# Optimization experiments

Hardware: AMD Instinct MI355X
Metric: run time of the kernel (lower is better)

The kernel has to match this reference:

```python
import jax, jax.numpy as jnp
import numpy as np

N = 50000
E = 300000
NEG_SLOPE = 0.2
EPS = 1e-16


def setup_inputs() -> dict:
    key = jax.random.key(0)
    ks = jax.random.split(key, 12)
    x = jax.random.normal(ks[0], (N, 27), dtype=jnp.float32)
    edge_index = jax.random.randint(ks[1], (2, E), 0, N, dtype=jnp.int64)
    # layer 1: in=27 -> heads1=4, dim=64
    W1 = jax.random.normal(ks[2], (27, 4 * 64), dtype=jnp.float32) * 0.1
    a_src1 = jax.random.normal(ks[3], (4, 64), dtype=jnp.float32) * 0.1
    a_dst1 = jax.random.normal(ks[4], (4, 64), dtype=jnp.float32) * 0.1
    b1 = jnp.zeros((4 * 64,), dtype=jnp.float32)
    # layer 2: in=256 -> heads2=2, dim=64
    W2 = jax.random.normal(ks[5], (256, 2 * 64), dtype=jnp.float32) * 0.05
    a_src2 = jax.random.normal(ks[6], (2, 64), dtype=jnp.float32) * 0.1
    a_dst2 = jax.random.normal(ks[7], (2, 64), dtype=jnp.float32) * 0.1
    b2 = jnp.zeros((2 * 64,), dtype=jnp.float32)
    # final linear: 128 -> 1
    Wfc = jax.random.normal(ks[8], (128, 1), dtype=jnp.float32) * 0.05
    bfc = jnp.zeros((1,), dtype=jnp.float32)
    return {"x": x, "edge_index": edge_index, "W1": W1, "a_src1": a_src1,
            "a_dst1": a_dst1, "b1": b1, "W2": W2, "a_src2": a_src2,
            "a_dst2": a_dst2, "b2": b2, "Wfc": Wfc, "bfc": bfc}


def gat_layer(x, src, dst, W, a_src, a_dst, b, heads, dim):
    # h: [N, H, D]
    h = (x @ W).reshape(N, heads, dim)
    # per-node attention half-scores: [N, H]
    s_src = jnp.einsum('nhd,hd->nh', h, a_src)
    s_dst = jnp.einsum('nhd,hd->nh', h, a_dst)
    # per-edge logits (gather) + leaky relu: [E', H]
    logits = jax.nn.leaky_relu(s_src[src] + s_dst[dst], negative_slope=NEG_SLOPE)
    # segment softmax over incoming edges at each destination node
    m = jax.ops.segment_max(logits, dst, num_segments=N)  # [N, H]
    m = jnp.where(jnp.isfinite(m), m, 0.0)
    e = jnp.exp(logits - m[dst])
    z = jax.ops.segment_sum(e, dst, num_segments=N)  # [N, H]
    alpha = e / (z[dst] + EPS)
    # weighted scatter-aggregate of source features
    out = jax.ops.segment_sum(h[src] * alpha[:, :, None], dst, num_segments=N)
    return out.reshape(N, heads * dim) + b


def reference(x, edge_index, W1, a_src1, a_dst1, b1, W2, a_src2, a_dst2, b2, Wfc, bfc):
    # add self-loops (PyG GATConv default add_self_loops=True)
    loops = jnp.arange(N, dtype=edge_index.dtype)
    src = jnp.concatenate([edge_index[0], loops])
    dst = jnp.concatenate([edge_index[1], loops])
    h = gat_layer(x, src, dst, W1, a_src1, a_dst1, b1, heads=4, dim=64)
    h = jax.nn.elu(h)
    h = gat_layer(h, src, dst, W2, a_src2, a_dst2, b2, heads=2, dim=64)
    h = jax.nn.elu(h)
    out = h @ Wfc + bfc
    return jax.nn.sigmoid(out)
```

## Files before the change

kernel.cpp:

```cpp
#include <hip/hip_runtime.h>
#include <math.h>

#define N_NODES 50000
#define E_EDGES 300000
#define E_TOT   350000
#define NEG 0.2f
#define EPS 1e-16f
#define CAP 32

typedef __attribute__((ext_vector_type(8))) short bf16x8;
typedef __attribute__((ext_vector_type(4))) float f32x4;

__device__ __forceinline__ float leaky(float x) { return x > 0.f ? x : NEG * x; }
__device__ __forceinline__ short f2bf(float v) {
    unsigned u = __float_as_uint(v);
    u += 0x7fffu + ((u >> 16) & 1u);
    return (short)(u >> 16);
}
__device__ __forceinline__ float bflo(unsigned u) { return __uint_as_float(u << 16); }
__device__ __forceinline__ float bfhi(unsigned u) { return __uint_as_float(u & 0xffff0000u); }
__device__ __forceinline__ unsigned bfpack(short a, short b) {
    return (unsigned)(unsigned short)a | ((unsigned)(unsigned short)b << 16);
}

__global__ __launch_bounds__(256) void k_scatter_s1(const int* __restrict__ ei,
        int* __restrict__ cnt, int* __restrict__ eidx,
        const float* __restrict__ x,
        const float* __restrict__ W1, const float* __restrict__ as1,
        const float* __restrict__ ad1, const float* __restrict__ W2,
        float* __restrict__ s1, short* __restrict__ xb,
        short* __restrict__ W1b, short* __restrict__ W2bT) {
    __shared__ float wsvL[216];
    int t = blockIdx.x * 256 + threadIdx.x;
    if (threadIdx.x < 216) {
        int k = threadIdx.x >> 3, j = threadIdx.x & 7;
        const float* av = (j < 4) ? (as1 + j * 64) : (ad1 + (j - 4) * 64);
        const float* wr = W1 + k * 256 + ((j & 3) * 64);
        float s = 0.f;
        #pragma unroll
        for (int d = 0; d < 64; ++d) s += wr[d] * av[d];
        wsvL[threadIdx.x] = s;
    }
    if (t < E_TOT) {
        int s = (t < E_EDGES) ? ei[t] : (t - E_EDGES);
        int d = (t < E_EDGES) ? ei[E_EDGES + t] : (t - E_EDGES);
        int pos = atomicAdd(&cnt[d], 1);
        if (pos < CAP) eidx[d * CAP + pos] = s;
    }
    if (t < 32768) {
        int col = t >> 8, k = t & 255;
        W2bT[t] = f2bf(W2[k * 128 + col]);
    }
    if (t < 8192) {
        int h = t >> 11, col = (t >> 5) & 63, k = t & 31;
        W1b[t] = f2bf(k < 27 ? W1[k * 256 + h * 64 + col] : 0.f);
    }
    __syncthreads();
    if (t < N_NODES * 8) {
        int n = t >> 3, j = t & 7;
        float s = 0.f;
        #pragma unroll
        for (int k = 0; k < 27; ++k) s += x[n * 27 + k] * wsvL[k * 8 + j];
        s1[t] = s;
        int c0 = j * 4;
        short p0 = f2bf(c0 + 0 < 27 ? x[n * 27 + c0 + 0] : 0.f);
        short p1 = f2bf(c0 + 1 < 27 ? x[n * 27 + c0 + 1] : 0.f);
        short p2 = f2bf(c0 + 2 < 27 ? x[n * 27 + c0 + 2] : 0.f);
        short p3 = f2bf(c0 + 3 < 27 ? x[n * 27 + c0 + 3] : 0.f);
        uint2 wv;
        wv.x = bfpack(p0, p1);
        wv.y = bfpack(p2, p3);
        *(uint2*)(xb + n * 32 + c0) = wv;
    }
}

__global__ __launch_bounds__(256) void k_fused1(const int* __restrict__ cnt,
        const int* __restrict__ eidx, const short* __restrict__ xb,
        const float* __restrict__ s1, const short* __restrict__ W1b,
        const short* __restrict__ W2bT, const float* __restrict__ b1,
        const float* __restrict__ as2, const float* __restrict__ ad2,
        short* __restrict__ h2b, float* __restrict__ s2) {
    __shared__ short LDSx[4 * 16 * 32];
    __shared__ short O[16 * 264];
    __shared__ float P[4][2][16];
    int w = threadIdx.x >> 6, l = threadIdx.x & 63;
    int n0 = blockIdx.x * 16;
    f32x4 z4 = {0.f, 0.f, 0.f, 0.f};

    {
        int g = threadIdx.x >> 4;
        int q = threadIdx.x & 15;
        int n = n0 + g;
        int beg = n * CAP;
        int espec = eidx[beg + q];
        int deg = min(cnt[n], CAP);
        int myi = (q < deg) ? espec : n;
        float4 sdv = *(const float4*)(s1 + n * 8 + 4);
        float a0 = 0.f, a1 = 0.f, a2 = 0.f, a3 = 0.f;
        float b0 = 0.f, b1v = 0.f, b2v = 0.f, b3 = 0.f;
        float z0 = 0.f, z1 = 0.f, z2 = 0.f, z3 = 0.f;
        float4 svq = *(const float4*)(s1 + myi * 8);
        float me0 = __expf(leaky(svq.x + sdv.x));
        float me1 = __expf(leaky(svq.y + sdv.y));
        float me2 = __expf(leaky(svq.z + sdv.z));
        float me3 = __expf(leaky(svq.w + sdv.w));
        int degw = deg;
        degw = max(degw, __shfl_xor(degw, 16));
        degw = max(degw, __shfl_xor(degw, 32));
        if (degw <= 16) {
            int lw = deg - 1;
            for (int i = 0; i < degw; i += 4) {
                bool m0 = i < deg, m1 = (i + 1) < deg;
                bool m2 = (i + 2) < deg, m3 = (i + 3) < deg;
                int j0 = m0 ? i : lw;
                int j1 = m1 ? i + 1 : lw;
                int j2 = m2 ? i + 2 : lw;
                int j3 = m3 ? i + 3 : lw;
                float g0 = m0 ? 1.f : 0.f, g1 = m1 ? 1.f : 0.f;
                float g2 = m2 ? 1.f : 0.f, g3 = m3 ? 1.f : 0.f;
                int s0 = __shfl(myi, j0, 16);
                int s1i = __shfl(myi, j1, 16);
                int s2i = __shfl(myi, j2, 16);
                int s3 = __shfl(myi, j3, 16);
                float e00 = g0 * __shfl(me0, j0, 16);
                float e01 = g0 * __shfl(me1, j0, 16);
                float e02 = g0 * __shfl(me2, j0, 16);
                float e03 = g0 * __shfl(me3, j0, 16);
                float e10 = g1 * __shfl(me0, j1, 16);
                float e11 = g1 * __shfl(me1, j1, 16);
                float e12 = g1 * __shfl(me2, j1, 16);
                float e13 = g1 * __shfl(me3, j1, 16);
                float e20 = g2 * __shfl(me0, j2, 16);
                float e21 = g2 * __shfl(me1, j2, 16);
                float e22 = g2 * __shfl(me2, j2, 16);
                float e23 = g2 * __shfl(me3, j2, 16);
                float e30 = g3 * __shfl(me0, j3, 16);
                float e31 = g3 * __shfl(me1, j3, 16);
                float e32 = g3 * __shfl(me2, j3, 16);
                float e33 = g3 * __shfl(me3, j3, 16);
                unsigned xv0 = *(const unsigned*)(xb + s0 * 32 + 2 * q);
                unsigned xv1 = *(const unsigned*)(xb + s1i * 32 + 2 * q);
                unsigned xv2 = *(const unsigned*)(xb + s2i * 32 + 2 * q);
                unsigned xv3 = *(const unsigned*)(xb + s3 * 32 + 2 * q);
                float xa0 = bflo(xv0), xc0 = bfhi(xv0);
                float xa1 = bflo(xv1), xc1 = bfhi(xv1);
                float xa2 = bflo(xv2), xc2 = bfhi(xv2);
                float xa3 = bflo(xv3), xc3 = bfhi(xv3);
                z0 += e00 + e10 + e20 + e30;
                z1 += e01 + e11 + e21 + e31;
                z2 += e02 + e12 + e22 + e32;
                z3 += e03 + e13 + e23 + e33;
                a0 += e00 * xa0 + e10 * xa1 + e20 * xa2 + e30 * xa3;
                a1 += e01 * xa0 + e11 * xa1 + e21 * xa2 + e31 * xa3;
                a2 += e02 * xa0 + e12 * xa1 + e22 * xa2 + e32 * xa3;
                a3 += e03 * xa0 + e13 * xa1 + e23 * xa2 + e33 * xa3;
                b0  += e00 * xc0 + e10 * xc1 + e20 * xc2 + e30 * xc3;
                b1v += e01 * xc0 + e11 * xc1 + e21 * xc2 + e31 * xc3;
                b2v += e02 * xc0 + e12 * xc1 + e22 * xc2 + e32 * xc3;
                b3  += e03 * xc0 + e13 * xc1 + e23 * xc2 + e33 * xc3;
            }
        } else {
            int last = beg + deg - 1;
            for (int i = 0; i < deg; i += 4) {
                bool m1 = (i + 1) < deg, m2 = (i + 2) < deg, m3 = (i + 3) < deg;
                int p0 = beg + i;
                int p1 = m1 ? p0 + 1 : last;
                int p2 = m2 ? p0 + 2 : last;
                int p3 = m3 ? p0 + 3 : last;
                int s0 = eidx[p0];
                int s1i = eidx[p1];
                int s2i = eidx[p2];
                int s3 = eidx[p3];
                float4 sv0 = *(const float4*)(s1 + s0 * 8);
                float4 sv1 = *(const float4*)(s1 + s1i * 8);
                float4 sv2 = *(const float4*)(s1 + s2i * 8);
                float4 sv3 = *(const float4*)(s1 + s3 * 8);
                unsigned xv0 = *(const unsigned*)(xb + s0 * 32 + 2 * q);
                unsigned xv1 = *(const unsigned*)(xb + s1i * 32 + 2 * q);
                unsigned xv2 = *(const unsigned*)(xb + s2i * 32 + 2 * q);
                unsigned xv3 = *(const unsigned*)(xb + s3 * 32 + 2 * q);
                float xa0 = bflo(xv0), xc0 = bfhi(xv0);
                float xa1 = bflo(xv1), xc1 = bfhi(xv1);
                float xa2 = bflo(xv2), xc2 = bfhi(xv2);
                float xa3 = bflo(xv3), xc3 = bfhi(xv3);
                float g1 = m1 ? 1.f : 0.f, g2 = m2 ? 1.f : 0.f, g3 = m3 ? 1.f : 0.f;
                float e00 = __expf(leaky(sv0.x + sdv.x));
                float e01 = __expf(leaky(sv0.y + sdv.y));
                float e02 = __expf(leaky(sv0.z + sdv.z));
                float e03 = __expf(leaky(sv0.w + sdv.w));
                float e10 = g1 * __expf(leaky(sv1.x + sdv.x));
                float e11 = g1 * __expf(leaky(sv1.y + sdv.y));
                float e12 = g1 * __expf(leaky(sv1.z + sdv.z));
                float e13 = g1 * __expf(leaky(sv1.w + sdv.w));
                float e20 = g2 * __expf(leaky(sv2.x + sdv.x));
                float e21 = g2 * __expf(leaky(sv2.y + sdv.y));
                float e22 = g2 * __expf(leaky(sv2.z + sdv.z));
                float e23 = g2 * __expf(leaky(sv2.w + sdv.w));
                float e30 = g3 * __expf(leaky(sv3.x + sdv.x));
                float e31 = g3 * __expf(leaky(sv3.y + sdv.y));
                float e32 = g3 * __expf(leaky(sv3.z + sdv.z));
                float e33 = g3 * __expf(leaky(sv3.w + sdv.w));
                z0 += e00 + e10 + e20 + e30;
                z1 += e01 + e11 + e21 + e31;
                z2 += e02 + e12 + e22 + e32;
                z3 += e03 + e13 + e23 + e33;
                a0 += e00 * xa0 + e10 * xa1 + e20 * xa2 + e30 * xa3;
                a1 += e01 * xa0 + e11 * xa1 + e21 * xa2 + e31 * xa3;
                a2 += e02 * xa0 + e12 * xa1 + e22 * xa2 + e32 * xa3;
                a3 += e03 * xa0 + e13 * xa1 + e23 * xa2 + e33 * xa3;
                b0  += e00 * xc0 + e10 * xc1 + e20 * xc2 + e30 * xc3;
                b1v += e01 * xc0 + e11 * xc1 + e21 * xc2 + e31 * xc3;
                b2v += e02 * xc0 + e12 * xc1 + e22 * xc2 + e32 * xc3;
                b3  += e03 * xc0 + e13 * xc1 + e23 * xc2 + e33 * xc3;
            }
        }
        float i0 = 1.f / (z0 + EPS), i1 = 1.f / (z1 + EPS);
        float i2 = 1.f / (z2 + EPS), i3 = 1.f / (z3 + EPS);
        int c2 = 2 * q;
        LDSx[0 * 512 + g * 32 + c2] = f2bf(a0 * i0);
        LDSx[1 * 512 + g * 32 + c2] = f2bf(a1 * i1);
        LDSx[2 * 512 + g * 32 + c2] = f2bf(a2 * i2);
        LDSx[3 * 512 + g * 32 + c2] = f2bf(a3 * i3);
        LDSx[0 * 512 + g * 32 + c2 + 1] = f2bf(b0 * i0);
        LDSx[1 * 512 + g * 32 + c2 + 1] = f2bf(b1v * i1);
        LDSx[2 * 512 + g * 32 + c2 + 1] = f2bf(b2v * i2);
        LDSx[3 * 512 + g * 32 + c2 + 1] = f2bf(b3 * i3);
    }
    __syncthreads();

    int lane16 = l & 15, quad = l >> 4;
    {
        bf16x8 a = *(const bf16x8*)&LDSx[w * 512 + lane16 * 32 + quad * 8];
        f32x4 cacc[4];
        #pragma unroll
        for (int nt = 0; nt < 4; ++nt) {
            bf16x8 b = *(const bf16x8*)&W1b[w * 2048 + (nt * 16 + lane16) * 32 + quad * 8];
            cacc[nt] = __builtin_amdgcn_mfma_f32_16x16x32_bf16(a, b, z4, 0, 0, 0);
        }
        #pragma unroll
        for (int nt = 0; nt < 4; ++nt) {
            int col = w * 64 + nt * 16 + lane16;
            float bb = b1[col];
            #pragma unroll
            for (int r2 = 0; r2 < 4; ++r2) {
                float v = cacc[nt][r2] + bb;
                v = v > 0.f ? v : __expf(v) - 1.f;
                O[(quad * 4 + r2) * 264 + col] = f2bf(v);
            }
        }
    }
    __syncthreads();

    f32x4 acc2[2];
    acc2[0] = z4; acc2[1] = z4;
    for (int k0 = 0; k0 < 256; k0 += 32) {
        bf16x8 a2 = *(const bf16x8*)&O[lane16 * 264 + k0 + quad * 8];
        #pragma unroll
        for (int j = 0; j < 2; ++j) {
            int ct = 2 * w + j;
            bf16x8 b2 = *(const bf16x8*)&W2bT[(ct * 16 + lane16) * 256 + k0 + quad * 8];
            acc2[j] = __builtin_amdgcn_mfma_f32_16x16x32_bf16(a2, b2, acc2[j], 0, 0, 0);
        }
    }
    float ps[4] = {0.f, 0.f, 0.f, 0.f}, pd[4] = {0.f, 0.f, 0.f, 0.f};
    #pragma unroll
    for (int j = 0; j < 2; ++j) {
        int col = (2 * w + j) * 16 + lane16;
        float a_s = as2[col], a_d = ad2[col];
        #pragma unroll
        for (int r2 = 0; r2 < 4; ++r2) {
            ps[r2] += acc2[j][r2] * a_s;
            pd[r2] += acc2[j][r2] * a_d;
            h2b[(n0 + quad * 4 + r2) * 128 + col] = f2bf(acc2[j][r2]);
        }
    }
    #pragma unroll
    for (int off = 1; off <= 8; off <<= 1)
        #pragma unroll
        for (int r2 = 0; r2 < 4; ++r2) {
            ps[r2] += __shfl_xor(ps[r2], off);
            pd[r2] += __shfl_xor(pd[r2], off);
        }
    if (lane16 == 0) {
        #pragma unroll
        for (int r2 = 0; r2 < 4; ++r2) {
            P[w][0][quad * 4 + r2] = ps[r2];
            P[w][1][quad * 4 + r2] = pd[r2];
        }
    }
    __syncthreads();
    if (threadIdx.x < 32) {
        int m = threadIdx.x & 15, hd = threadIdx.x >> 4;
        s2[(n0 + m) * 4 + hd]     = P[2 * hd][0][m] + P[2 * hd + 1][0][m];
        s2[(n0 + m) * 4 + 2 + hd] = P[2 * hd][1][m] + P[2 * hd + 1][1][m];
    }
}

__global__ __launch_bounds__(256) void k_agg2_csr(const int* __restrict__ cnt,
        const int* __restrict__ eidx, const float* __restrict__ s2,
        const short* __restrict__ h2b, const float* __restrict__ b2,
        const float* __restrict__ Wfc, const float* __restrict__ bfc,
        float* __restrict__ out) {
    int g = threadIdx.x >> 4;
    int q = threadIdx.x & 15;
    int n = blockIdx.x * 16 + g;
    int beg = n * CAP;
    int espec = eidx[beg + q];
    int deg = min(cnt[n], CAP);
    int myi = (q < deg) ? espec : n;
    int h = q >> 3;
    float2 sdv = *(const float2*)(s2 + n * 4 + 2);
    float4 accA = make_float4(0.f, 0.f, 0.f, 0.f);
    float4 accB = make_float4(0.f, 0.f, 0.f, 0.f);
    float z = 0.f;
    float2 svq = *(const float2*)(s2 + myi * 4);
    float mea = __expf(leaky(svq.x + sdv.x));
    float meb = __expf(leaky(svq.y + sdv.y));
    int degw = deg;
    degw = max(degw, __shfl_xor(degw, 16));
    degw = max(degw, __shfl_xor(degw, 32));
    if (degw <= 16) {
        int lw = deg - 1;
        for (int i = 0; i < degw; i += 4) {
            bool m0 = i < deg, m1 = (i + 1) < deg;
            bool m2 = (i + 2) < deg, m3 = (i + 3) < deg;
            int j0 = m0 ? i : lw;
            int j1 = m1 ? i + 1 : lw;
            int j2 = m2 ? i + 2 : lw;
            int j3 = m3 ? i + 3 : lw;
            int a0 = __shfl(myi, j0, 16);
            int a1 = __shfl(myi, j1, 16);
            int a2 = __shfl(myi, j2, 16);
            int a3 = __shfl(myi, j3, 16);
            float ea0 = __shfl(mea, j0, 16), eb0 = __shfl(meb, j0, 16);
            float ea1 = __shfl(mea, j1, 16), eb1 = __shfl(meb, j1, 16);
            float ea2 = __shfl(mea, j2, 16), eb2 = __shfl(meb, j2, 16);
            float ea3 = __shfl(mea, j3, 16), eb3 = __shfl(meb, j3, 16);
            float e0 = (m0 ? 1.f : 0.f) * (h ? eb0 : ea0);
            float e1 = (m1 ? 1.f : 0.f) * (h ? eb1 : ea1);
            float e2 = (m2 ? 1.f : 0.f) * (h ? eb2 : ea2);
            float e3 = (m3 ? 1.f : 0.f) * (h ? eb3 : ea3);
            uint4 v0 = *(const uint4*)(h2b + a0 * 128 + q * 8);
            uint4 v1 = *(const uint4*)(h2b + a1 * 128 + q * 8);
            uint4 v2 = *(const uint4*)(h2b + a2 * 128 + q * 8);
            uint4 v3 = *(const uint4*)(h2b + a3 * 128 + q * 8);
            z += e0 + e1 + e2 + e3;
            accA.x += e0 * bflo(v0.x) + e1 * bflo(v1.x) + e2 * bflo(v2.x) + e3 * bflo(v3.x);
            accA.y += e0 * bfhi(v0.x) + e1 * bfhi(v1.x) + e2 * bfhi(v2.x) + e3 * bfhi(v3.x);
            accA.z += e0 * bflo(v0.y) + e1 * bflo(v1.y) + e2 * bflo(v2.y) + e3 * bflo(v3.y);
            accA.w += e0 * bfhi(v0.y) + e1 * bfhi(v1.y) + e2 * bfhi(v2.y) + e3 * bfhi(v3.y);
            accB.x += e0 * bflo(v0.z) + e1 * bflo(v1.z) + e2 * bflo(v2.z) + e3 * bflo(v3.z);
            accB.y += e0 * bfhi(v0.z) + e1 * bfhi(v1.z) + e2 * bfhi(v2.z) + e3 * bfhi(v3.z);
            accB.z += e0 * bflo(v0.w) + e1 * bflo(v1.w) + e2 * bflo(v2.w) + e3 * bflo(v3.w);
            accB.w += e0 * bfhi(v0.w) + e1 * bfhi(v1.w) + e2 * bfhi(v2.w) + e3 * bfhi(v3.w);
        }
    } else {
        float sd = h ? sdv.y : sdv.x;
        int i = 0;
        for (; i + 4 <= deg; i += 4) {
            int a0 = eidx[beg + i], a1 = eidx[beg + i + 1];
            int a2 = eidx[beg + i + 2], a3 = eidx[beg + i + 3];
            float e0 = __expf(leaky(s2[a0 * 4 + h] + sd));
            float e1 = __expf(leaky(s2[a1 * 4 + h] + sd));
            float e2 = __expf(leaky(s2[a2 * 4 + h] + sd));
            float e3 = __expf(leaky(s2[a3 * 4 + h] + sd));
            uint4 v0 = *(const uint4*)(h2b + a0 * 128 + q * 8);
            uint4 v1 = *(const uint4*)(h2b + a1 * 128 + q * 8);
            uint4 v2 = *(const uint4*)(h2b + a2 * 128 + q * 8);
            uint4 v3 = *(const uint4*)(h2b + a3 * 128 + q * 8);
            z += e0 + e1 + e2 + e3;
            accA.x += e0 * bflo(v0.x) + e1 * bflo(v1.x) + e2 * bflo(v2.x) + e3 * bflo(v3.x);
            accA.y += e0 * bfhi(v0.x) + e1 * bfhi(v1.x) + e2 * bfhi(v2.x) + e3 * bfhi(v3.x);
            accA.z += e0 * bflo(v0.y) + e1 * bflo(v1.y) + e2 * bflo(v2.y) + e3 * bflo(v3.y);
            accA.w += e0 * bfhi(v0.y) + e1 * bfhi(v1.y) + e2 * bfhi(v2.y) + e3 * bfhi(v3.y);
            accB.x += e0 * bflo(v0.z) + e1 * bflo(v1.z) + e2 * bflo(v2.z) + e3 * bflo(v3.z);
            accB.y += e0 * bfhi(v0.z) + e1 * bfhi(v1.z) + e2 * bfhi(v2.z) + e3 * bfhi(v3.z);
            accB.z += e0 * bflo(v0.w) + e1 * bflo(v1.w) + e2 * bflo(v2.w) + e3 * bflo(v3.w);
            accB.w += e0 * bfhi(v0.w) + e1 * bfhi(v1.w) + e2 * bfhi(v2.w) + e3 * bfhi(v3.w);
        }
        for (; i < deg; ++i) {
            int a0 = eidx[beg + i];
            float e0 = __expf(leaky(s2[a0 * 4 + h] + sd));
            uint4 v0 = *(const uint4*)(h2b + a0 * 128 + q * 8);
            z += e0;
            accA.x += e0 * bflo(v0.x); accA.y += e0 * bfhi(v0.x);
            accA.z += e0 * bflo(v0.y); accA.w += e0 * bfhi(v0.y);
            accB.x += e0 * bflo(v0.z); accB.y += e0 * bfhi(v0.z);
            accB.z += e0 * bflo(v0.w); accB.w += e0 * bfhi(v0.w);
        }
    }
    float inv = 1.f / (z + EPS);
    int c0 = q * 8;
    float p = 0.f;
    float va[8] = {accA.x, accA.y, accA.z, accA.w, accB.x, accB.y, accB.z, accB.w};
    #pragma unroll
    for (int j = 0; j < 8; ++j) {
        float v = va[j] * inv + b2[c0 + j];
        v = v > 0.f ? v : __expf(v) - 1.f;
        p += v * Wfc[c0 + j];
    }
    #pragma unroll
    for (int off = 1; off <= 8; off <<= 1) p += __shfl_xor(p, off);
    if (q == 0) out[n] = 1.f / (1.f + __expf(-(p + bfc[0])));
}

extern "C" void kernel_launch(void* const* d_in, const int* in_sizes, int n_in,
                              void* d_out, int out_size, void* d_ws, size_t ws_size,
                              hipStream_t stream) {
    const float* x   = (const float*)d_in[0];
    const int*   ei  = (const int*)d_in[1];
    const float* W1  = (const float*)d_in[2];
    const float* as1 = (const float*)d_in[3];
    const float* ad1 = (const float*)d_in[4];
    const float* b1  = (const float*)d_in[5];
    const float* W2  = (const float*)d_in[6];
    const float* as2 = (const float*)d_in[7];
    const float* ad2 = (const float*)d_in[8];
    const float* b2  = (const float*)d_in[9];
    const float* Wfc = (const float*)d_in[10];
    const float* bfc = (const float*)d_in[11];
    float* out = (float*)d_out;

    float* f = (float*)d_ws;
    short* h2b   = (short*)f;
    float* s1    = f + 3200000;
    float* s2    = f + 3600000;
    int*   cnt   = (int*)(f + 3810000);
    int*   eidx  = (int*)(f + 3870000);
    short* W1b   = (short*)(f + 5500000);
    short* W2bT  = (short*)(f + 5510000);
    short* xb    = (short*)(f + 5530000);

    hipMemsetAsync(cnt, 0, N_NODES * sizeof(int), stream);

    k_scatter_s1<<<1563, 256, 0, stream>>>(ei, cnt, eidx, x, W1, as1, ad1, W2,
                                           s1, xb, W1b, W2bT);

    k_fused1<<<3125, 256, 0, stream>>>(cnt, eidx, xb, s1, W1b, W2bT, b1,
                                       as2, ad2, h2b, s2);

    k_agg2_csr<<<3125, 256, 0, stream>>>(cnt, eidx, s2, h2b, b2, Wfc, bfc, out);
}
```

Baseline: 168.9 us.

## Split fused layer-1 kernel into gather kernel and 32-row MFMA dense kernel

The fused kernel that gathered neighbour features and then ran both MFMA GEMMs is split in two. The gather kernel writes the normalized per-head aggregates to a padded global bf16 buffer. The dense kernel then processes 32 nodes per block, so each W1/W2 fragment load feeds two MFMAs. This decouples the latency-bound gather from the compute-bound dense work and improves weight reuse. In exchange it adds an extra kernel launch and a global round trip for the aggregated features, plus padding writes.

```diff
diff --git a/kernel.cpp b/kernel.cpp
--- a/kernel.cpp
+++ b/kernel.cpp
@@ -2,11 +2,13 @@
 #include <math.h>
 
 #define N_NODES 50000
+#define N_PAD   50016
 #define E_EDGES 300000
 #define E_TOT   350000
 #define NEG 0.2f
 #define EPS 1e-16f
 #define CAP 32
+#define PLANE (N_PAD * 32)
 
 typedef __attribute__((ext_vector_type(8))) short bf16x8;
 typedef __attribute__((ext_vector_type(4))) float f32x4;
@@ -74,168 +76,174 @@
     }
 }
 
-__global__ __launch_bounds__(256) void k_fused1(const int* __restrict__ cnt,
+__global__ __launch_bounds__(256) void k_gather1(const int* __restrict__ cnt,
         const int* __restrict__ eidx, const short* __restrict__ xb,
-        const float* __restrict__ s1, const short* __restrict__ W1b,
-        const short* __restrict__ W2bT, const float* __restrict__ b1,
-        const float* __restrict__ as2, const float* __restrict__ ad2,
-        short* __restrict__ h2b, float* __restrict__ s2) {
-    __shared__ short LDSx[4 * 16 * 32];
-    __shared__ short O[16 * 264];
-    __shared__ float P[4][2][16];
+        const float* __restrict__ s1, short* __restrict__ xagg) {
+    int g = threadIdx.x >> 4;
+    int q = threadIdx.x & 15;
+    int n = blockIdx.x * 16 + g;
+    int c2 = 2 * q;
+    if (n >= N_NODES) {
+        if (n < N_PAD) {
+            *(unsigned*)(xagg + 0 * PLANE + n * 32 + c2) = 0u;
+            *(unsigned*)(xagg + 1 * PLANE + n * 32 + c2) = 0u;
+            *(unsigned*)(xagg + 2 * PLANE + n * 32 + c2) = 0u;
+            *(unsigned*)(xagg + 3 * PLANE + n * 32 + c2) = 0u;
+        }
+        return;
+    }
+    int beg = n * CAP;
+    int espec = eidx[beg + q];
+    int deg = min(cnt[n], CAP);
+    int myi = (q < deg) ? espec : n;
+    float4 sdv = *(const float4*)(s1 + n * 8 + 4);
+    float a0 = 0.f, a1 = 0.f, a2 = 0.f, a3 = 0.f;
+    float b0 = 0.f, b1v = 0.f, b2v = 0.f, b3 = 0.f;
+    float z0 = 0.f, z1 = 0.f, z2 = 0.f, z3 = 0.f;
+    float4 svq = *(const float4*)(s1 + myi * 8);
+    float me0 = __expf(leaky(svq.x + sdv.x));
+    float me1 = __expf(leaky(svq.y + sdv.y));
+    float me2 = __expf(leaky(svq.z + sdv.z));
+    float me3 = __expf(leaky(svq.w + sdv.w));
+    int degw = deg;
+    degw = max(degw, __shfl_xor(degw, 16));
+    degw = max(degw, __shfl_xor(degw, 32));
+    if (degw <= 16) {
+        int lw = deg - 1;
+        for (int i = 0; i < degw; i += 4) {
+            bool m0 = i < deg, m1 = (i + 1) < deg;
+            bool m2 = (i + 2) < deg, m3 = (i + 3) < deg;
+            int j0 = m0 ? i : lw;
+            int j1 = m1 ? i + 1 : lw;
+            int j2 = m2 ? i + 2 : lw;
+            int j3 = m3 ? i + 3 : lw;
+            float g0 = m0 ? 1.f : 0.f, g1 = m1 ? 1.f : 0.f;
+            float g2 = m2 ? 1.f : 0.f, g3 = m3 ? 1.f : 0.f;
+            int s0 = __shfl(myi, j0, 16);
+            int s1i = __shfl(myi, j1, 16);
+            int s2i = __shfl(myi, j2, 16);
+            int s3 = __shfl(myi, j3, 16);
+            float e00 = g0 * __shfl(me0, j0, 16);
+            float e01 = g0 * __shfl(me1, j0, 16);
+            float e02 = g0 * __shfl(me2, j0, 16);
+            float e03 = g0 * __shfl(me3, j0, 16);
+            float e10 = g1 * __shfl(me0, j1, 16);
+            float e11 = g1 * __shfl(me1, j1, 16);
+            float e12 = g1 * __shfl(me2, j1, 16);
+            float e13 = g1 * __shfl(me3, j1, 16);
+            float e20 = g2 * __shfl(me0, j2, 16);
+            float e21 = g2 * __shfl(me1, j2, 16);
+            float e22 = g2 * __shfl(me2, j2, 16);
+            float e23 = g2 * __shfl(me3, j2, 16);
+            float e30 = g3 * __shfl(me0, j3, 16);
+            float e31 = g3 * __shfl(me1, j3, 16);
+            float e32 = g3 * __shfl(me2, j3, 16);
+            float e33 = g3 * __shfl(me3, j3, 16);
+            unsigned xv0 = *(const unsigned*)(xb + s0 * 32 + 2 * q);
+            unsigned xv1 = *(const unsigned*)(xb + s1i * 32 + 2 * q);
+            unsigned xv2 = *(const unsigned*)(xb + s2i * 32 + 2 * q);
+            unsigned xv3 = *(const unsigned*)(xb + s3 * 32 + 2 * q);
+            float xa0 = bflo(xv0), xc0 = bfhi(xv0);
+            float xa1 = bflo(xv1), xc1 = bfhi(xv1);
+            float xa2 = bflo(xv2), xc2 = bfhi(xv2);
+            float xa3 = bflo(xv3), xc3 = bfhi(xv3);
+            z0 += e00 + e10 + e20 + e30;
+            z1 += e01 + e11 + e21 + e31;
+            z2 += e02 + e12 + e22 + e32;
+            z3 += e03 + e13 + e23 + e33;
+            a0 += e00 * xa0 + e10 * xa1 + e20 * xa2 + e30 * xa3;
+            a1 += e01 * xa0 + e11 * xa1 + e21 * xa2 + e31 * xa3;
+            a2 += e02 * xa0 + e12 * xa1 + e22 * xa2 + e32 * xa3;
+            a3 += e03 * xa0 + e13 * xa1 + e23 * xa2 + e33 * xa3;
+            b0  += e00 * xc0 + e10 * xc1 + e20 * xc2 + e30 * xc3;
+            b1v += e01 * xc0 + e11 * xc1 + e21 * xc2 + e31 * xc3;
+            b2v += e02 * xc0 + e12 * xc1 + e22 * xc2 + e32 * xc3;
+            b3  += e03 * xc0 + e13 * xc1 + e23 * xc2 + e33 * xc3;
+        }
+    } else {
+        int last = beg + deg - 1;
+        for (int i = 0; i < deg; i += 4) {
+            bool m1 = (i + 1) < deg, m2 = (i + 2) < deg, m3 = (i + 3) < deg;
+            int p0 = beg + i;
+            int p1 = m1 ? p0 + 1 : last;
+            int p2 = m2 ? p0 + 2 : last;
+            int p3 = m3 ? p0 + 3 : last;
+            int s0 = eidx[p0];
+            int s1i = eidx[p1];
+            int s2i = eidx[p2];
+            int s3 = eidx[p3];
+            float4 sv0 = *(const float4*)(s1 + s0 * 8);
+            float4 sv1 = *(const float4*)(s1 + s1i * 8);
+            float4 sv2 = *(const float4*)(s1 + s2i * 8);
+            float4 sv3 = *(const float4*)(s1 + s3 * 8);
+            unsigned xv0 = *(const unsigned*)(xb + s0 * 32 + 2 * q);
+            unsigned xv1 = *(const unsigned*)(xb + s1i * 32 + 2 * q);
+            unsigned xv2 = *(const unsigned*)(xb + s2i * 32 + 2 * q);
+            unsigned xv3 = *(const unsigned*)(xb + s3 * 32 + 2 * q);
+            float xa0 = bflo(xv0), xc0 = bfhi(xv0);
+            float xa1 = bflo(xv1), xc1 = bfhi(xv1);
+            float xa2 = bflo(xv2), xc2 = bfhi(xv2);
+            float xa3 = bflo(xv3), xc3 = bfhi(xv3);
+            float g1 = m1 ? 1.f : 0.f, g2 = m2 ? 1.f : 0.f, g3 = m3 ? 1.f : 0.f;
+            float e00 = __expf(leaky(sv0.x + sdv.x));
+            float e01 = __expf(leaky(sv0.y + sdv.y));
+            float e02 = __expf(leaky(sv0.z + sdv.z));
+            float e03 = __expf(leaky(sv0.w + sdv.w));
+            float e10 = g1 * __expf(leaky(sv1.x + sdv.x));
+            float e11 = g1 * __expf(leaky(sv1.y + sdv.y));
+            float e12 = g1 * __expf(leaky(sv1.z + sdv.z));
+            float e13 = g1 * __expf(leaky(sv1.w + sdv.w));
+            float e20 = g2 * __expf(leaky(sv2.x + sdv.x));
+            float e21 = g2 * __expf(leaky(sv2.y + sdv.y));
+            float e22 = g2 * __expf(leaky(sv2.z + sdv.z));
+            float e23 = g2 * __expf(leaky(sv2.w + sdv.w));
+            float e30 = g3 * __expf(leaky(sv3.x + sdv.x));
+            float e31 = g3 * __expf(leaky(sv3.y + sdv.y));
+            float e32 = g3 * __expf(leaky(sv3.z + sdv.z));
+            float e33 = g3 * __expf(leaky(sv3.w + sdv.w));
+            z0 += e00 + e10 + e20 + e30;
+            z1 += e01 + e11 + e21 + e31;
+            z2 += e02 + e12 + e22 + e32;
+            z3 += e03 + e13 + e23 + e33;
+            a0 += e00 * xa0 + e10 * xa1 + e20 * xa2 + e30 * xa3;
+            a1 += e01 * xa0 + e11 * xa1 + e21 * xa2 + e31 * xa3;
+            a2 += e02 * xa0 + e12 * xa1 + e22 * xa2 + e32 * xa3;
+            a3 += e03 * xa0 + e13 * xa1 + e23 * xa2 + e33 * xa3;
+            b0  += e00 * xc0 + e10 * xc1 + e20 * xc2 + e30 * xc3;
+            b1v += e01 * xc0 + e11 * xc1 + e21 * xc2 + e31 * xc3;
+            b2v += e02 * xc0 + e12 * xc1 + e22 * xc2 + e32 * xc3;
+            b3  += e03 * xc0 + e13 * xc1 + e23 * xc2 + e33 * xc3;
+        }
+    }
+    float i0 = 1.f / (z0 + EPS), i1 = 1.f / (z1 + EPS);
+    float i2 = 1.f / (z2 + EPS), i3 = 1.f / (z3 + EPS);
+    *(unsigned*)(xagg + 0 * PLANE + n * 32 + c2) = bfpack(f2bf(a0 * i0), f2bf(b0 * i0));
+    *(unsigned*)(xagg + 1 * PLANE + n * 32 + c2) = bfpack(f2bf(a1 * i1), f2bf(b1v * i1));
+    *(unsigned*)(xagg + 2 * PLANE + n * 32 + c2) = bfpack(f2bf(a2 * i2), f2bf(b2v * i2));
+    *(unsigned*)(xagg + 3 * PLANE + n * 32 + c2) = bfpack(f2bf(a3 * i3), f2bf(b3 * i3));
+}
+
+__global__ __launch_bounds__(256) void k_dense(const short* __restrict__ xagg,
+        const short* __restrict__ W1b, const short* __restrict__ W2bT,
+        const float* __restrict__ b1, const float* __restrict__ as2,
+        const float* __restrict__ ad2, short* __restrict__ h2b,
+        float* __restrict__ s2) {
+    __shared__ short O[32 * 264];
+    __shared__ float P[4][2][32];
     int w = threadIdx.x >> 6, l = threadIdx.x & 63;
-    int n0 = blockIdx.x * 16;
+    int lane16 = l & 15, quad = l >> 4;
+    int n0 = blockIdx.x * 32;
     f32x4 z4 = {0.f, 0.f, 0.f, 0.f};
 
     {
-        int g = threadIdx.x >> 4;
-        int q = threadIdx.x & 15;
-        int n = n0 + g;
-        int beg = n * CAP;
-        int espec = eidx[beg + q];
-        int deg = min(cnt[n], CAP);
-        int myi = (q < deg) ? espec : n;
-        float4 sdv = *(const float4*)(s1 + n * 8 + 4);
-        float a0 = 0.f, a1 = 0.f, a2 = 0.f, a3 = 0.f;
-        float b0 = 0.f, b1v = 0.f, b2v = 0.f, b3 = 0.f;
-        float z0 = 0.f, z1 = 0.f, z2 = 0.f, z3 = 0.f;
-        float4 svq = *(const float4*)(s1 + myi * 8);
-        float me0 = __expf(leaky(svq.x + sdv.x));
-        float me1 = __expf(leaky(svq.y + sdv.y));
-        float me2 = __expf(leaky(svq.z + sdv.z));
-        float me3 = __expf(leaky(svq.w + sdv.w));
-        int degw = deg;
-        degw = max(degw, __shfl_xor(degw, 16));
-        degw = max(degw, __shfl_xor(degw, 32));
-        if (degw <= 16) {
-            int lw = deg - 1;
-            for (int i = 0; i < degw; i += 4) {
-                bool m0 = i < deg, m1 = (i + 1) < deg;
-                bool m2 = (i + 2) < deg, m3 = (i + 3) < deg;
-                int j0 = m0 ? i : lw;
-                int j1 = m1 ? i + 1 : lw;
-                int j2 = m2 ? i + 2 : lw;
-                int j3 = m3 ? i + 3 : lw;
-                float g0 = m0 ? 1.f : 0.f, g1 = m1 ? 1.f : 0.f;
-                float g2 = m2 ? 1.f : 0.f, g3 = m3 ? 1.f : 0.f;
-                int s0 = __shfl(myi, j0, 16);
-                int s1i = __shfl(myi, j1, 16);
-                int s2i = __shfl(myi, j2, 16);
-                int s3 = __shfl(myi, j3, 16);
-                float e00 = g0 * __shfl(me0, j0, 16);
-                float e01 = g0 * __shfl(me1, j0, 16);
-                float e02 = g0 * __shfl(me2, j0, 16);
-                float e03 = g0 * __shfl(me3, j0, 16);
-                float e10 = g1 * __shfl(me0, j1, 16);
-                float e11 = g1 * __shfl(me1, j1, 16);
-                float e12 = g1 * __shfl(me2, j1, 16);
-                float e13 = g1 * __shfl(me3, j1, 16);
-                float e20 = g2 * __shfl(me0, j2, 16);
-                float e21 = g2 * __shfl(me1, j2, 16);
-                float e22 = g2 * __shfl(me2, j2, 16);
-                float e23 = g2 * __shfl(me3, j2, 16);
-                float e30 = g3 * __shfl(me0, j3, 16);
-                float e31 = g3 * __shfl(me1, j3, 16);
-                float e32 = g3 * __shfl(me2, j3, 16);
-                float e33 = g3 * __shfl(me3, j3, 16);
-                unsigned xv0 = *(const unsigned*)(xb + s0 * 32 + 2 * q);
-                unsigned xv1 = *(const unsigned*)(xb + s1i * 32 + 2 * q);
-                unsigned xv2 = *(const unsigned*)(xb + s2i * 32 + 2 * q);
-                unsigned xv3 = *(const unsigned*)(xb + s3 * 32 + 2 * q);
-                float xa0 = bflo(xv0), xc0 = bfhi(xv0);
-                float xa1 = bflo(xv1), xc1 = bfhi(xv1);
-                float xa2 = bflo(xv2), xc2 = bfhi(xv2);
-                float xa3 = bflo(xv3), xc3 = bfhi(xv3);
-                z0 += e00 + e10 + e20 + e30;
-                z1 += e01 + e11 + e21 + e31;
-                z2 += e02 + e12 + e22 + e32;
-                z3 += e03 + e13 + e23 + e33;
-                a0 += e00 * xa0 + e10 * xa1 + e20 * xa2 + e30 * xa3;
-                a1 += e01 * xa0 + e11 * xa1 + e21 * xa2 + e31 * xa3;
-                a2 += e02 * xa0 + e12 * xa1 + e22 * xa2 + e32 * xa3;
-                a3 += e03 * xa0 + e13 * xa1 + e23 * xa2 + e33 * xa3;
-                b0  += e00 * xc0 + e10 * xc1 + e20 * xc2 + e30 * xc3;
-                b1v += e01 * xc0 + e11 * xc1 + e21 * xc2 + e31 * xc3;
-                b2v += e02 * xc0 + e12 * xc1 + e22 * xc2 + e32 * xc3;
-                b3  += e03 * xc0 + e13 * xc1 + e23 * xc2 + e33 * xc3;
-            }
-        } else {
-            int last = beg + deg - 1;
-            for (int i = 0; i < deg; i += 4) {
-                bool m1 = (i + 1) < deg, m2 = (i + 2) < deg, m3 = (i + 3) < deg;
-                int p0 = beg + i;
-                int p1 = m1 ? p0 + 1 : last;
-                int p2 = m2 ? p0 + 2 : last;
-                int p3 = m3 ? p0 + 3 : last;
-                int s0 = eidx[p0];
-                int s1i = eidx[p1];
-                int s2i = eidx[p2];
-                int s3 = eidx[p3];
-                float4 sv0 = *(const float4*)(s1 + s0 * 8);
-                float4 sv1 = *(const float4*)(s1 + s1i * 8);
-                float4 sv2 = *(const float4*)(s1 + s2i * 8);
-                float4 sv3 = *(const float4*)(s1 + s3 * 8);
-                unsigned xv0 = *(const unsigned*)(xb + s0 * 32 + 2 * q);
-                unsigned xv1 = *(const unsigned*)(xb + s1i * 32 + 2 * q);
-                unsigned xv2 = *(const unsigned*)(xb + s2i * 32 + 2 * q);
-                unsigned xv3 = *(const unsigned*)(xb + s3 * 32 + 2 * q);
-                float xa0 = bflo(xv0), xc0 = bfhi(xv0);
-                float xa1 = bflo(xv1), xc1 = bfhi(xv1);
-                float xa2 = bflo(xv2), xc2 = bfhi(xv2);
-                float xa3 = bflo(xv3), xc3 = bfhi(xv3);
-                float g1 = m1 ? 1.f : 0.f, g2 = m2 ? 1.f : 0.f, g3 = m3 ? 1.f : 0.f;
-                float e00 = __expf(leaky(sv0.x + sdv.x));
-                float e01 = __expf(leaky(sv0.y + sdv.y));
-                float e02 = __expf(leaky(sv0.z + sdv.z));
-                float e03 = __expf(leaky(sv0.w + sdv.w));
-                float e10 = g1 * __expf(leaky(sv1.x + sdv.x));
-                float e11 = g1 * __expf(leaky(sv1.y + sdv.y));
-                float e12 = g1 * __expf(leaky(sv1.z + sdv.z));
-                float e13 = g1 * __expf(leaky(sv1.w + sdv.w));
-                float e20 = g2 * __expf(leaky(sv2.x + sdv.x));
-                float e21 = g2 * __expf(leaky(sv2.y + sdv.y));
-                float e22 = g2 * __expf(leaky(sv2.z + sdv.z));
-                float e23 = g2 * __expf(leaky(sv2.w + sdv.w));
-                float e30 = g3 * __expf(leaky(sv3.x + sdv.x));
-                float e31 = g3 * __expf(leaky(sv3.y + sdv.y));
-                float e32 = g3 * __expf(leaky(sv3.z + sdv.z));
-                float e33 = g3 * __expf(leaky(sv3.w + sdv.w));
-                z0 += e00 + e10 + e20 + e30;
-                z1 += e01 + e11 + e21 + e31;
-                z2 += e02 + e12 + e22 + e32;
-                z3 += e03 + e13 + e23 + e33;
-                a0 += e00 * xa0 + e10 * xa1 + e20 * xa2 + e30 * xa3;
-                a1 += e01 * xa0 + e11 * xa1 + e21 * xa2 + e31 * xa3;
-                a2 += e02 * xa0 + e12 * xa1 + e22 * xa2 + e32 * xa3;
-                a3 += e03 * xa0 + e13 * xa1 + e23 * xa2 + e33 * xa3;
-                b0  += e00 * xc0 + e10 * xc1 + e20 * xc2 + e30 * xc3;
-                b1v += e01 * xc0 + e11 * xc1 + e21 * xc2 + e31 * xc3;
-                b2v += e02 * xc0 + e12 * xc1 + e22 * xc2 + e32 * xc3;
-                b3  += e03 * xc0 + e13 * xc1 + e23 * xc2 + e33 * xc3;
-            }
-        }
-        float i0 = 1.f / (z0 + EPS), i1 = 1.f / (z1 + EPS);
-        float i2 = 1.f / (z2 + EPS), i3 = 1.f / (z3 + EPS);
-        int c2 = 2 * q;
-        LDSx[0 * 512 + g * 32 + c2] = f2bf(a0 * i0);
-        LDSx[1 * 512 + g * 32 + c2] = f2bf(a1 * i1);
-        LDSx[2 * 512 + g * 32 + c2] = f2bf(a2 * i2);
-        LDSx[3 * 512 + g * 32 + c2] = f2bf(a3 * i3);
-        LDSx[0 * 512 + g * 32 + c2 + 1] = f2bf(b0 * i0);
-        LDSx[1 * 512 + g * 32 + c2 + 1] = f2bf(b1v * i1);
-        LDSx[2 * 512 + g * 32 + c2 + 1] = f2bf(b2v * i2);
-        LDSx[3 * 512 + g * 32 + c2 + 1] = f2bf(b3 * i3);
-    }
-    __syncthreads();
-
-    int lane16 = l & 15, quad = l >> 4;
-    {
-        bf16x8 a = *(const bf16x8*)&LDSx[w * 512 + lane16 * 32 + quad * 8];
-        f32x4 cacc[4];
+        bf16x8 am0 = *(const bf16x8*)&xagg[w * PLANE + (n0 + lane16) * 32 + quad * 8];
+        bf16x8 am1 = *(const bf16x8*)&xagg[w * PLANE + (n0 + 16 + lane16) * 32 + quad * 8];
+        f32x4 c0[4], c1[4];
         #pragma unroll
         for (int nt = 0; nt < 4; ++nt) {
             bf16x8 b = *(const bf16x8*)&W1b[w * 2048 + (nt * 16 + lane16) * 32 + quad * 8];
-            cacc[nt] = __builtin_amdgcn_mfma_f32_16x16x32_bf16(a, b, z4, 0, 0, 0);
+            c0[nt] = __builtin_amdgcn_mfma_f32_16x16x32_bf16(am0, b, z4, 0, 0, 0);
+            c1[nt] = __builtin_amdgcn_mfma_f32_16x16x32_bf16(am1, b, z4, 0, 0, 0);
         }
         #pragma unroll
         for (int nt = 0; nt < 4; ++nt) {
@@ -243,56 +251,73 @@
             float bb = b1[col];
             #pragma unroll
             for (int r2 = 0; r2 < 4; ++r2) {
-                float v = cacc[nt][r2] + bb;
+                float v = c0[nt][r2] + bb;
                 v = v > 0.f ? v : __expf(v) - 1.f;
                 O[(quad * 4 + r2) * 264 + col] = f2bf(v);
+                float u = c1[nt][r2] + bb;
+                u = u > 0.f ? u : __expf(u) - 1.f;
+                O[(16 + quad * 4 + r2) * 264 + col] = f2bf(u);
             }
         }
     }
     __syncthreads();
 
-    f32x4 acc2[2];
-    acc2[0] = z4; acc2[1] = z4;
+    f32x4 acc[2][2];
+    acc[0][0] = z4; acc[0][1] = z4; acc[1][0] = z4; acc[1][1] = z4;
     for (int k0 = 0; k0 < 256; k0 += 32) {
-        bf16x8 a2 = *(const bf16x8*)&O[lane16 * 264 + k0 + quad * 8];
+        bf16x8 a0 = *(const bf16x8*)&O[lane16 * 264 + k0 + quad * 8];
+        bf16x8 a1 = *(const bf16x8*)&O[(16 + lane16) * 264 + k0 + quad * 8];
         #pragma unroll
         for (int j = 0; j < 2; ++j) {
             int ct = 2 * w + j;
             bf16x8 b2 = *(const bf16x8*)&W2bT[(ct * 16 + lane16) * 256 + k0 + quad * 8];
-            acc2[j] = __builtin_amdgcn_mfma_f32_16x16x32_bf16(a2, b2, acc2[j], 0, 0, 0);
-        }
-    }
-    float ps[4] = {0.f, 0.f, 0.f, 0.f}, pd[4] = {0.f, 0.f, 0.f, 0.f};
+            acc[0][j] = __builtin_amdgcn_mfma_f32_16x16x32_bf16(a0, b2, acc[0][j], 0, 0, 0);
+            acc[1][j] = __builtin_amdgcn_mfma_f32_16x16x32_bf16(a1, b2, acc[1][j], 0, 0, 0);
+        }
+    }
+    float ps[2][4] = {{0.f,0.f,0.f,0.f},{0.f,0.f,0.f,0.f}};
+    float pd[2][4] = {{0.f,0.f,0.f,0.f},{0.f,0.f,0.f,0.f}};
     #pragma unroll
     for (int j = 0; j < 2; ++j) {
         int col = (2 * w + j) * 16 + lane16;
         float a_s = as2[col], a_d = ad2[col];
         #pragma unroll
-        for (int r2 = 0; r2 < 4; ++r2) {
-            ps[r2] += acc2[j][r2] * a_s;
-            pd[r2] += acc2[j][r2] * a_d;
-            h2b[(n0 + quad * 4 + r2) * 128 + col] = f2bf(acc2[j][r2]);
+        for (int m = 0; m < 2; ++m) {
+            #pragma unroll
+            for (int r2 = 0; r2 < 4; ++r2) {
+                ps[m][r2] += acc[m][j][r2] * a_s;
+                pd[m][r2] += acc[m][j][r2] * a_d;
+                int row = n0 + m * 16 + quad * 4 + r2;
+                if (row < N_NODES) h2b[row * 128 + col] = f2bf(acc[m][j][r2]);
+            }
         }
     }
     #pragma unroll
     for (int off = 1; off <= 8; off <<= 1)
         #pragma unroll
-        for (int r2 = 0; r2 < 4; ++r2) {
-            ps[r2] += __shfl_xor(ps[r2], off);
-            pd[r2] += __shfl_xor(pd[r2], off);
-        }
+        for (int m = 0; m < 2; ++m)
+            #pragma unroll
+            for (int r2 = 0; r2 < 4; ++r2) {
+                ps[m][r2] += __shfl_xor(ps[m][r2], off);
+                pd[m][r2] += __shfl_xor(pd[m][r2], off);
+            }
     if (lane16 == 0) {
         #pragma unroll
-        for (int r2 = 0; r2 < 4; ++r2) {
-            P[w][0][quad * 4 + r2] = ps[r2];
-            P[w][1][quad * 4 + r2] = pd[r2];
-        }
+        for (int m = 0; m < 2; ++m)
+            #pragma unroll
+            for (int r2 = 0; r2 < 4; ++r2) {
+                P[w][0][m * 16 + quad * 4 + r2] = ps[m][r2];
+                P[w][1][m * 16 + quad * 4 + r2] = pd[m][r2];
+            }
     }
     __syncthreads();
-    if (threadIdx.x < 32) {
-        int m = threadIdx.x & 15, hd = threadIdx.x >> 4;
-        s2[(n0 + m) * 4 + hd]     = P[2 * hd][0][m] + P[2 * hd + 1][0][m];
-        s2[(n0 + m) * 4 + 2 + hd] = P[2 * hd][1][m] + P[2 * hd + 1][1][m];
+    if (threadIdx.x < 64) {
+        int m = threadIdx.x & 31, hd = threadIdx.x >> 5;
+        int row = n0 + m;
+        if (row < N_NODES) {
+            s2[row * 4 + hd]     = P[2 * hd][0][m] + P[2 * hd + 1][0][m];
+            s2[row * 4 + 2 + hd] = P[2 * hd][1][m] + P[2 * hd + 1][1][m];
+        }
     }
 }
 
@@ -430,14 +455,16 @@
     short* W1b   = (short*)(f + 5500000);
     short* W2bT  = (short*)(f + 5510000);
     short* xb    = (short*)(f + 5530000);
+    short* xagg  = (short*)(f + 6400000);
 
     hipMemsetAsync(cnt, 0, N_NODES * sizeof(int), stream);
 
     k_scatter_s1<<<1563, 256, 0, stream>>>(ei, cnt, eidx, x, W1, as1, ad1, W2,
                                            s1, xb, W1b, W2bT);
 
-    k_fused1<<<3125, 256, 0, stream>>>(cnt, eidx, xb, s1, W1b, W2bT, b1,
-                                       as2, ad2, h2b, s2);
+    k_gather1<<<3126, 256, 0, stream>>>(cnt, eidx, xb, s1, xagg);
+
+    k_dense<<<1563, 256, 0, stream>>>(xagg, W1b, W2bT, b1, as2, ad2, h2b, s2);
 
     k_agg2_csr<<<3125, 256, 0, stream>>>(cnt, eidx, s2, h2b, b2, Wfc, bfc, out);
 }
```

Result: no change. 167.7 us (-0.7%).
